# Performance work log

Hardware: AMD Instinct MI355X
Metric: run time of the kernel (lower is better)

The kernel has to match this reference:

```python
import jax, jax.numpy as jnp
import numpy as np

N = 8192
FEAT = 3
TRIG = 2
SA = 2
H = 64
ACT = 3
NEG = -1.0e9
EPS = 1e-5


def setup_inputs() -> dict:
    key = jax.random.key(0)
    ks = jax.random.split(key, 24)
    s = 0.05
    node_features = jax.random.uniform(ks[0], (N, FEAT), dtype=jnp.float32)
    adj = jax.random.randint(ks[1], (N, N), 0, 2).astype(jnp.float32)
    # ensure self-loops so every row has at least one neighbor
    adj_matrix = jnp.maximum(adj, jnp.eye(N, dtype=jnp.float32))
    trigger_context = jax.random.uniform(ks[2], (TRIG,), dtype=jnp.float32)
    sa_priors = jax.random.normal(ks[3], (N, SA), dtype=jnp.float32)
    p = lambda k, sh: jax.random.normal(k, sh, dtype=jnp.float32) * s
    return {
        "node_features": node_features,
        "adj_matrix": adj_matrix,
        "trigger_context": trigger_context,
        "sa_priors": sa_priors,
        # node_encoder: Linear(5,64) -> ReLU -> Linear(64,64)
        "w1": p(ks[4], (FEAT + TRIG, H)), "b1": jnp.zeros((H,), jnp.float32),
        "w2": p(ks[5], (H, H)), "b2": jnp.zeros((H,), jnp.float32),
        "wq": p(ks[6], (H, H)), "bq": jnp.zeros((H,), jnp.float32),
        "wk": p(ks[7], (H, H)), "bk": jnp.zeros((H,), jnp.float32),
        "wg": p(ks[8], (TRIG, H)), "bg": jnp.zeros((H,), jnp.float32),
        "stateful_bias": jnp.zeros((1,), jnp.float32),
        "wm": p(ks[9], (H, H)), "bm": jnp.zeros((H,), jnp.float32),
        "ln_g": jnp.ones((H,), jnp.float32), "ln_b": jnp.zeros((H,), jnp.float32),
        "wa1": p(ks[10], (H + SA, H)), "ba1": jnp.zeros((H,), jnp.float32),
        "wa2": p(ks[11], (H, ACT)), "ba2": jnp.zeros((ACT,), jnp.float32),
    }


def reference(node_features, adj_matrix, trigger_context, sa_priors,
              w1, b1, w2, b2, wq, bq, wk, bk, wg, bg, stateful_bias,
              wm, bm, ln_g, ln_b, wa1, ba1, wa2, ba2):
    n = node_features.shape[0]
    trig = jnp.broadcast_to(trigger_context[None, :], (n, TRIG))
    x = jnp.concatenate([node_features, trig], axis=1)          # [N, 5]
    h = jax.nn.relu(x @ w1 + b1) @ w2 + b2                       # [N, H]
    q = h @ wq + bq
    k = h @ wk + bk
    scores = (q @ k.T) * (1.0 / np.sqrt(H))                      # [N, N]
    gate_factor = jnp.mean(jax.nn.sigmoid(trigger_context @ wg + bg))
    topo = jnp.where(adj_matrix == 0, jnp.float32(NEG), adj_matrix)
    is_stateful = node_features[:, 2]
    is_reactive = 1.0 - trigger_context[0]
    sb = jnp.outer(is_stateful, is_stateful) * (stateful_bias[0] * is_reactive)
    scores = scores * gate_factor + topo + sb
    attn = jax.nn.softmax(scores, axis=1)                        # [N, N]
    messages = h @ wm + bm
    aggregated = attn @ messages                                 # [N, H]
    z = h + aggregated
    mu = jnp.mean(z, axis=-1, keepdims=True)
    var = jnp.mean(jnp.square(z - mu), axis=-1, keepdims=True)
    emb = (z - mu) * jax.lax.rsqrt(var + EPS) * ln_g + ln_b      # LayerNorm
    ai = jnp.concatenate([emb, sa_priors], axis=1)               # [N, H+2]
    q_values = jax.nn.relu(ai @ wa1 + ba1) @ wa2 + ba2           # [N, 3]
    return q_values
```

## Files before the change

kernel.cpp:

```cpp
#include <hip/hip_runtime.h>
#include <hip/hip_bf16.h>
#include <math.h>

#define N 8192
#define NEGV -1000000000.0f
#define EPSV 1e-05f
#define NSPLIT 4
#define CPS (N / NSPLIT)
#define NTILE (CPS / 64)

typedef short bf16x8 __attribute__((ext_vector_type(8)));
typedef float f32x4 __attribute__((ext_vector_type(4)));
typedef unsigned short u16;

#define WS_SCAL 0
#define WS_H    64
#define WS_ST   (WS_H + N * 64)
#define WS_SBI  (WS_ST + N)
#define WS_DEN  (WS_SBI + N)
#define WS_AGG  (WS_DEN + NSPLIT * N)
#define WS_F_END (WS_AGG + NSPLIT * N * 64)
#define WU_BASE (WS_F_END * 2)
#define WU_QB (WU_BASE)
#define WU_KB (WU_BASE + N * 64)
#define WU_MB (WU_BASE + 2 * N * 64)
#define WU_MT (WU_BASE + 3 * N * 64)

static __device__ __forceinline__ u16 f2bf(float f) {
    __hip_bfloat16 h = __float2bfloat16(f);
    return *(u16*)&h;
}

__global__ void prep_k(const float* __restrict__ tc, const float* __restrict__ wg,
                       const float* __restrict__ bg, const float* __restrict__ sbias,
                       float* __restrict__ scal) {
    int j = threadIdx.x;
    float v = tc[0] * wg[j] + tc[1] * wg[64 + j] + bg[j];
    float g = 1.0f / (1.0f + __expf(-v));
    for (int off = 32; off; off >>= 1) g += __shfl_xor(g, off, 64);
    if (j == 0) {
        scal[0] = 0.125f * (g * (1.0f / 64.0f));
        scal[1] = sbias[0] * (1.0f - tc[0]);
    }
}

__global__ __launch_bounds__(256) void embed_k(
    const float* __restrict__ nf, const float* __restrict__ tc,
    const float* __restrict__ w1, const float* __restrict__ b1,
    const float* __restrict__ w2, const float* __restrict__ b2,
    const float* __restrict__ wq, const float* __restrict__ bq,
    const float* __restrict__ wk, const float* __restrict__ bk,
    const float* __restrict__ wm, const float* __restrict__ bm,
    float* __restrict__ ws)
{
    const int w = threadIdx.x >> 6, lane = threadIdx.x & 63;
    const int row = blockIdx.x * 4 + w;
    __shared__ float ts[4][64], hs[4][64];
    const float qscale = ws[WS_SCAL + 0];
    const float coef   = ws[WS_SCAL + 1];
    const float f0 = nf[row * 3], f1 = nf[row * 3 + 1], f2 = nf[row * 3 + 2];
    const float t0 = tc[0], t1 = tc[1];
    float v = b1[lane];
    v = fmaf(f0, w1[lane], v);
    v = fmaf(f1, w1[64 + lane], v);
    v = fmaf(f2, w1[128 + lane], v);
    v = fmaf(t0, w1[192 + lane], v);
    v = fmaf(t1, w1[256 + lane], v);
    ts[w][lane] = fmaxf(v, 0.0f);
    __syncthreads();
    float hv = b2[lane];
    #pragma unroll 8
    for (int j = 0; j < 64; j++) hv = fmaf(ts[w][j], w2[j * 64 + lane], hv);
    hs[w][lane] = hv;
    ws[WS_H + row * 64 + lane] = hv;
    __syncthreads();
    float qv = bq[lane], kv = bk[lane], mv = bm[lane];
    #pragma unroll 4
    for (int j = 0; j < 64; j++) {
        const float hj = hs[w][j];
        qv = fmaf(hj, wq[j * 64 + lane], qv);
        kv = fmaf(hj, wk[j * 64 + lane], kv);
        mv = fmaf(hj, wm[j * 64 + lane], mv);
    }
    u16* wu = (u16*)ws;
    wu[WU_QB + row * 64 + lane] = f2bf(qv * qscale);
    wu[WU_KB + row * 64 + lane] = f2bf(kv);
    wu[WU_MB + row * 64 + lane] = f2bf(mv);
    if (lane == 0) {
        ws[WS_ST + row]  = f2;
        ws[WS_SBI + row] = f2 * coef;
    }
}

__global__ __launch_bounds__(256) void transp_k(float* __restrict__ ws) {
    const u16* mb = (const u16*)ws + WU_MB;
    u16* mt = (u16*)ws + WU_MT;
    __shared__ __align__(16) u16 tile[64][72];
    const int i0 = blockIdx.x * 64;
    const int t = threadIdx.x;
    {
        const int r = t >> 2, cb = (t & 3) * 16;
        *(uint4*)&tile[r][cb]     = *(const uint4*)&mb[(size_t)(i0 + r) * 64 + cb];
        *(uint4*)&tile[r][cb + 8] = *(const uint4*)&mb[(size_t)(i0 + r) * 64 + cb + 8];
    }
    __syncthreads();
    const int c = t >> 2, rb = (t & 3) * 16;
    u16 tmp[16];
    #pragma unroll
    for (int i = 0; i < 16; i++) tmp[i] = tile[rb + i][c];
    *(uint4*)&mt[(size_t)c * N + i0 + rb]     = *(uint4*)&tmp[0];
    *(uint4*)&mt[(size_t)c * N + i0 + rb + 8] = *(uint4*)&tmp[8];
}

__global__ __launch_bounds__(256, 2) void attn_k(const float* __restrict__ adj,
                                                 float* __restrict__ ws)
{
    const int rb = blockIdx.x, sp = blockIdx.y;
    const int i0 = rb * 64, j0 = sp * CPS;
    const int tid = threadIdx.x;
    const int w = tid >> 6, lane = tid & 63;
    const int quad = lane >> 4, n16 = lane & 15;
    const int m0 = w * 16;

    __shared__ __align__(16) u16 qs[64][72];
    __shared__ __align__(16) u16 ks[2][64][72];
    __shared__ __align__(16) u16 ms[2][64][72];
    __shared__ __align__(16) u16 ps[64][72];
    __shared__ float sts[2][64];
    __shared__ float sbis[64];

    const u16* qb = (const u16*)ws + WU_QB;
    const u16* kb = (const u16*)ws + WU_KB;
    const u16* mt = (const u16*)ws + WU_MT;

    const int sr = tid >> 2, scb = (tid & 3) * 16;

    *(uint4*)&qs[sr][scb]     = *(const uint4*)&qb[(size_t)(i0 + sr) * 64 + scb];
    *(uint4*)&qs[sr][scb + 8] = *(const uint4*)&qb[(size_t)(i0 + sr) * 64 + scb + 8];
    if (tid < 64) sbis[tid] = ws[WS_SBI + i0 + tid];
    {
        const int jt = j0;
        *(uint4*)&ks[0][sr][scb]     = *(const uint4*)&kb[(size_t)(jt + sr) * 64 + scb];
        *(uint4*)&ks[0][sr][scb + 8] = *(const uint4*)&kb[(size_t)(jt + sr) * 64 + scb + 8];
        *(uint4*)&ms[0][sr][scb]     = *(const uint4*)&mt[(size_t)sr * N + jt + scb];
        *(uint4*)&ms[0][sr][scb + 8] = *(const uint4*)&mt[(size_t)sr * N + jt + scb + 8];
        if (tid < 64) sts[0][tid] = ws[WS_ST + jt + tid];
    }
    __syncthreads();

    const bf16x8 aq0 = *(const bf16x8*)&qs[m0 + n16][quad * 8];
    const bf16x8 aq1 = *(const bf16x8*)&qs[m0 + n16][32 + quad * 8];

    f32x4 acc[4];
    #pragma unroll
    for (int i = 0; i < 4; i++) acc[i] = (f32x4){0.f, 0.f, 0.f, 0.f};
    float den[4] = {0.f, 0.f, 0.f, 0.f};
    float sbr[4];
    #pragma unroll
    for (int v = 0; v < 4; v++) sbr[v] = sbis[m0 + quad * 4 + v];

    for (int t = 0; t < NTILE; t++) {
        const int cur = t & 1;
        const int jt = j0 + t * 64;

        float aa[4][4];
        #pragma unroll
        for (int reg = 0; reg < 4; reg++) {
            const size_t rowb = (size_t)(i0 + m0 + quad * 4 + reg) * N + jt + n16;
            #pragma unroll
            for (int ct = 0; ct < 4; ct++) aa[ct][reg] = adj[rowb + ct * 16];
        }

        if (t + 1 < NTILE) {
            const int jn = jt + 64;
            *(uint4*)&ks[cur ^ 1][sr][scb]     = *(const uint4*)&kb[(size_t)(jn + sr) * 64 + scb];
            *(uint4*)&ks[cur ^ 1][sr][scb + 8] = *(const uint4*)&kb[(size_t)(jn + sr) * 64 + scb + 8];
            *(uint4*)&ms[cur ^ 1][sr][scb]     = *(const uint4*)&mt[(size_t)sr * N + jn + scb];
            *(uint4*)&ms[cur ^ 1][sr][scb + 8] = *(const uint4*)&mt[(size_t)sr * N + jn + scb + 8];
            if (tid < 64) sts[cur ^ 1][tid] = ws[WS_ST + jn + tid];
        }

        #pragma unroll
        for (int ct = 0; ct < 4; ct++) {
            const bf16x8 b0 = *(const bf16x8*)&ks[cur][ct * 16 + n16][quad * 8];
            const bf16x8 b1 = *(const bf16x8*)&ks[cur][ct * 16 + n16][32 + quad * 8];
            f32x4 s = {0.f, 0.f, 0.f, 0.f};
            s = __builtin_amdgcn_mfma_f32_16x16x32_bf16(aq0, b0, s, 0, 0, 0);
            s = __builtin_amdgcn_mfma_f32_16x16x32_bf16(aq1, b1, s, 0, 0, 0);
            const float stc = sts[cur][ct * 16 + n16];
            #pragma unroll
            for (int reg = 0; reg < 4; reg++) {
                const float a = aa[ct][reg];
                const float sc = s[reg] + (a == 0.0f ? NEGV : a) + sbr[reg] * stc;
                const float p = __expf(sc);
                den[reg] += p;
                ps[m0 + quad * 4 + reg][ct * 16 + n16] = f2bf(p);
            }
        }
        __syncthreads();

        const bf16x8 ap0 = *(const bf16x8*)&ps[m0 + n16][quad * 8];
        const bf16x8 ap1 = *(const bf16x8*)&ps[m0 + n16][32 + quad * 8];
        #pragma unroll
        for (int nt = 0; nt < 4; nt++) {
            const bf16x8 b0 = *(const bf16x8*)&ms[cur][nt * 16 + n16][quad * 8];
            const bf16x8 b1 = *(const bf16x8*)&ms[cur][nt * 16 + n16][32 + quad * 8];
            acc[nt] = __builtin_amdgcn_mfma_f32_16x16x32_bf16(ap0, b0, acc[nt], 0, 0, 0);
            acc[nt] = __builtin_amdgcn_mfma_f32_16x16x32_bf16(ap1, b1, acc[nt], 0, 0, 0);
        }
        __syncthreads();
    }

    float* aggp = ws + WS_AGG + (size_t)sp * N * 64;
    #pragma unroll
    for (int nt = 0; nt < 4; nt++) {
        #pragma unroll
        for (int reg = 0; reg < 4; reg++) {
            aggp[(size_t)(i0 + m0 + quad * 4 + reg) * 64 + nt * 16 + n16] = acc[nt][reg];
        }
    }
    #pragma unroll
    for (int reg = 0; reg < 4; reg++) {
        float d = den[reg];
        d += __shfl_xor(d, 1, 64);
        d += __shfl_xor(d, 2, 64);
        d += __shfl_xor(d, 4, 64);
        d += __shfl_xor(d, 8, 64);
        if (n16 == 0) ws[WS_DEN + sp * N + i0 + m0 + quad * 4 + reg] = d;
    }
}

__global__ __launch_bounds__(256) void final_k(
    const float* __restrict__ sa, const float* __restrict__ ln_g,
    const float* __restrict__ ln_b,
    const float* __restrict__ wa1, const float* __restrict__ ba1,
    const float* __restrict__ wa2, const float* __restrict__ ba2,
    const float* __restrict__ ws, float* __restrict__ out)
{
    const int w = threadIdx.x >> 6, lane = threadIdx.x & 63;
    const int row = blockIdx.x * 4 + w;
    __shared__ float es[4][64], hs2[4][64];
    float a = 0.0f;
    #pragma unroll
    for (int sp = 0; sp < NSPLIT; sp++)
        a += ws[WS_AGG + (size_t)sp * N * 64 + (size_t)row * 64 + lane];
    float d = 0.0f;
    #pragma unroll
    for (int sp = 0; sp < NSPLIT; sp++) d += ws[WS_DEN + sp * N + row];
    const float z = ws[WS_H + row * 64 + lane] + a / d;
    float mu = z;
    for (int off = 32; off; off >>= 1) mu += __shfl_xor(mu, off, 64);
    mu *= (1.0f / 64.0f);
    const float zc = z - mu;
    float var = zc * zc;
    for (int off = 32; off; off >>= 1) var += __shfl_xor(var, off, 64);
    var *= (1.0f / 64.0f);
    const float emb = zc * rsqrtf(var + EPSV) * ln_g[lane] + ln_b[lane];
    es[w][lane] = emb;
    __syncthreads();
    const float sa0 = sa[row * 2], sa1 = sa[row * 2 + 1];
    float hv = ba1[lane];
    #pragma unroll 8
    for (int c = 0; c < 64; c++) hv = fmaf(es[w][c], wa1[c * 64 + lane], hv);
    hv = fmaf(sa0, wa1[64 * 64 + lane], hv);
    hv = fmaf(sa1, wa1[65 * 64 + lane], hv);
    hs2[w][lane] = fmaxf(hv, 0.0f);
    __syncthreads();
    if (lane < 3) {
        float o = ba2[lane];
        for (int u = 0; u < 64; u++) o = fmaf(hs2[w][u], wa2[u * 3 + lane], o);
        out[row * 3 + lane] = o;
    }
}

extern "C" void kernel_launch(void* const* d_in, const int* in_sizes, int n_in,
                              void* d_out, int out_size, void* d_ws, size_t ws_size,
                              hipStream_t stream)
{
    const float* nf  = (const float*)d_in[0];
    const float* adj = (const float*)d_in[1];
    const float* tc  = (const float*)d_in[2];
    const float* sa  = (const float*)d_in[3];
    const float* w1  = (const float*)d_in[4];
    const float* b1  = (const float*)d_in[5];
    const float* w2  = (const float*)d_in[6];
    const float* b2  = (const float*)d_in[7];
    const float* wq  = (const float*)d_in[8];
    const float* bq  = (const float*)d_in[9];
    const float* wk  = (const float*)d_in[10];
    const float* bk  = (const float*)d_in[11];
    const float* wg  = (const float*)d_in[12];
    const float* bg  = (const float*)d_in[13];
    const float* sb  = (const float*)d_in[14];
    const float* wm  = (const float*)d_in[15];
    const float* bm  = (const float*)d_in[16];
    const float* lng = (const float*)d_in[17];
    const float* lnb = (const float*)d_in[18];
    const float* wa1 = (const float*)d_in[19];
    const float* ba1 = (const float*)d_in[20];
    const float* wa2 = (const float*)d_in[21];
    const float* ba2 = (const float*)d_in[22];
    float* ws  = (float*)d_ws;
    float* out = (float*)d_out;

    prep_k<<<1, 64, 0, stream>>>(tc, wg, bg, sb, ws + WS_SCAL);
    embed_k<<<N / 4, 256, 0, stream>>>(nf, tc, w1, b1, w2, b2, wq, bq, wk, bk,
                                       wm, bm, ws);
    transp_k<<<N / 64, 256, 0, stream>>>(ws);
    attn_k<<<dim3(N / 64, NSPLIT), 256, 0, stream>>>(adj, ws);
    final_k<<<N / 4, 256, 0, stream>>>(sa, lng, lnb, wa1, ba1, wa2, ba2, ws, out);
}
```

Measured before the change: 474.2 us.

## Register-prefetch K/M and adjacency tiles, single-buffer LDS, double the column splits

```diff
diff --git a/kernel.cpp b/kernel.cpp
--- a/kernel.cpp
+++ b/kernel.cpp
@@ -5,7 +5,7 @@
 #define N 8192
 #define NEGV -1000000000.0f
 #define EPSV 1e-05f
-#define NSPLIT 4
+#define NSPLIT 8
 #define CPS (N / NSPLIT)
 #define NTILE (CPS / 64)
 
@@ -112,85 +112,102 @@
     *(uint4*)&mt[(size_t)c * N + i0 + rb + 8] = *(uint4*)&tmp[8];
 }
 
-__global__ __launch_bounds__(256, 2) void attn_k(const float* __restrict__ adj,
+__global__ __launch_bounds__(256, 3) void attn_k(const float* __restrict__ adj,
                                                  float* __restrict__ ws)
 {
     const int rb = blockIdx.x, sp = blockIdx.y;
     const int i0 = rb * 64, j0 = sp * CPS;
     const int tid = threadIdx.x;
-    const int w = tid >> 6, lane = tid & 63;
+    const int lane = tid & 63;
     const int quad = lane >> 4, n16 = lane & 15;
-    const int m0 = w * 16;
-
-    __shared__ __align__(16) u16 qs[64][72];
-    __shared__ __align__(16) u16 ks[2][64][72];
-    __shared__ __align__(16) u16 ms[2][64][72];
+    const int m0 = (tid >> 6) * 16;
+
+    __shared__ __align__(16) u16 ks[64][72];
+    __shared__ __align__(16) u16 ms[64][72];
     __shared__ __align__(16) u16 ps[64][72];
-    __shared__ float sts[2][64];
-    __shared__ float sbis[64];
 
     const u16* qb = (const u16*)ws + WU_QB;
     const u16* kb = (const u16*)ws + WU_KB;
     const u16* mt = (const u16*)ws + WU_MT;
+    const float* st_g = ws + WS_ST;
 
     const int sr = tid >> 2, scb = (tid & 3) * 16;
 
-    *(uint4*)&qs[sr][scb]     = *(const uint4*)&qb[(size_t)(i0 + sr) * 64 + scb];
-    *(uint4*)&qs[sr][scb + 8] = *(const uint4*)&qb[(size_t)(i0 + sr) * 64 + scb + 8];
-    if (tid < 64) sbis[tid] = ws[WS_SBI + i0 + tid];
+    uint4 kmA[2][4];
+    float aaR[2][4][4];
+    float stR[2][4];
+
     {
         const int jt = j0;
-        *(uint4*)&ks[0][sr][scb]     = *(const uint4*)&kb[(size_t)(jt + sr) * 64 + scb];
-        *(uint4*)&ks[0][sr][scb + 8] = *(const uint4*)&kb[(size_t)(jt + sr) * 64 + scb + 8];
-        *(uint4*)&ms[0][sr][scb]     = *(const uint4*)&mt[(size_t)sr * N + jt + scb];
-        *(uint4*)&ms[0][sr][scb + 8] = *(const uint4*)&mt[(size_t)sr * N + jt + scb + 8];
-        if (tid < 64) sts[0][tid] = ws[WS_ST + jt + tid];
-    }
-    __syncthreads();
-
-    const bf16x8 aq0 = *(const bf16x8*)&qs[m0 + n16][quad * 8];
-    const bf16x8 aq1 = *(const bf16x8*)&qs[m0 + n16][32 + quad * 8];
-
-    f32x4 acc[4];
-    #pragma unroll
-    for (int i = 0; i < 4; i++) acc[i] = (f32x4){0.f, 0.f, 0.f, 0.f};
-    float den[4] = {0.f, 0.f, 0.f, 0.f};
-    float sbr[4];
-    #pragma unroll
-    for (int v = 0; v < 4; v++) sbr[v] = sbis[m0 + quad * 4 + v];
-
-    for (int t = 0; t < NTILE; t++) {
-        const int cur = t & 1;
-        const int jt = j0 + t * 64;
-
-        float aa[4][4];
+        uint4 k0 = *(const uint4*)&kb[(size_t)(jt + sr) * 64 + scb];
+        uint4 k1 = *(const uint4*)&kb[(size_t)(jt + sr) * 64 + scb + 8];
+        uint4 q0 = *(const uint4*)&mt[(size_t)sr * N + jt + scb];
+        uint4 q1 = *(const uint4*)&mt[(size_t)sr * N + jt + scb + 8];
         #pragma unroll
         for (int reg = 0; reg < 4; reg++) {
             const size_t rowb = (size_t)(i0 + m0 + quad * 4 + reg) * N + jt + n16;
             #pragma unroll
-            for (int ct = 0; ct < 4; ct++) aa[ct][reg] = adj[rowb + ct * 16];
-        }
-
-        if (t + 1 < NTILE) {
-            const int jn = jt + 64;
-            *(uint4*)&ks[cur ^ 1][sr][scb]     = *(const uint4*)&kb[(size_t)(jn + sr) * 64 + scb];
-            *(uint4*)&ks[cur ^ 1][sr][scb + 8] = *(const uint4*)&kb[(size_t)(jn + sr) * 64 + scb + 8];
-            *(uint4*)&ms[cur ^ 1][sr][scb]     = *(const uint4*)&mt[(size_t)sr * N + jn + scb];
-            *(uint4*)&ms[cur ^ 1][sr][scb + 8] = *(const uint4*)&mt[(size_t)sr * N + jn + scb + 8];
-            if (tid < 64) sts[cur ^ 1][tid] = ws[WS_ST + jn + tid];
+            for (int ct = 0; ct < 4; ct++) aaR[0][ct][reg] = adj[rowb + ct * 16];
+        }
+        #pragma unroll
+        for (int ct = 0; ct < 4; ct++) stR[0][ct] = st_g[jt + ct * 16 + n16];
+        const int j1 = j0 + ((NTILE > 1) ? 64 : 0);
+        kmA[1][0] = *(const uint4*)&kb[(size_t)(j1 + sr) * 64 + scb];
+        kmA[1][1] = *(const uint4*)&kb[(size_t)(j1 + sr) * 64 + scb + 8];
+        kmA[1][2] = *(const uint4*)&mt[(size_t)sr * N + j1 + scb];
+        kmA[1][3] = *(const uint4*)&mt[(size_t)sr * N + j1 + scb + 8];
+        *(uint4*)&ks[sr][scb]     = k0;
+        *(uint4*)&ks[sr][scb + 8] = k1;
+        *(uint4*)&ms[sr][scb]     = q0;
+        *(uint4*)&ms[sr][scb + 8] = q1;
+    }
+
+    const bf16x8 aq0 = *(const bf16x8*)&qb[(size_t)(i0 + m0 + n16) * 64 + quad * 8];
+    const bf16x8 aq1 = *(const bf16x8*)&qb[(size_t)(i0 + m0 + n16) * 64 + 32 + quad * 8];
+    float sbr[4];
+    #pragma unroll
+    for (int v = 0; v < 4; v++) sbr[v] = ws[WS_SBI + i0 + m0 + quad * 4 + v];
+
+    f32x4 acc[4];
+    #pragma unroll
+    for (int i = 0; i < 4; i++) acc[i] = (f32x4){0.f, 0.f, 0.f, 0.f};
+    float den[4] = {0.f, 0.f, 0.f, 0.f};
+
+    __syncthreads();
+
+    #pragma unroll 2
+    for (int t = 0; t < NTILE; t++) {
+        const int cur = t & 1, nxt = 1 - cur;
+        {
+            const int tk = (t + 2 < NTILE) ? t + 2 : NTILE - 1;
+            const int jk = j0 + tk * 64;
+            kmA[cur][0] = *(const uint4*)&kb[(size_t)(jk + sr) * 64 + scb];
+            kmA[cur][1] = *(const uint4*)&kb[(size_t)(jk + sr) * 64 + scb + 8];
+            kmA[cur][2] = *(const uint4*)&mt[(size_t)sr * N + jk + scb];
+            kmA[cur][3] = *(const uint4*)&mt[(size_t)sr * N + jk + scb + 8];
+            const int ta = (t + 1 < NTILE) ? t + 1 : NTILE - 1;
+            const int ja = j0 + ta * 64;
+            #pragma unroll
+            for (int reg = 0; reg < 4; reg++) {
+                const size_t rowb = (size_t)(i0 + m0 + quad * 4 + reg) * N + ja + n16;
+                #pragma unroll
+                for (int ct = 0; ct < 4; ct++) aaR[nxt][ct][reg] = adj[rowb + ct * 16];
+            }
+            #pragma unroll
+            for (int ct = 0; ct < 4; ct++) stR[nxt][ct] = st_g[ja + ct * 16 + n16];
         }
 
         #pragma unroll
         for (int ct = 0; ct < 4; ct++) {
-            const bf16x8 b0 = *(const bf16x8*)&ks[cur][ct * 16 + n16][quad * 8];
-            const bf16x8 b1 = *(const bf16x8*)&ks[cur][ct * 16 + n16][32 + quad * 8];
+            const bf16x8 b0 = *(const bf16x8*)&ks[ct * 16 + n16][quad * 8];
+            const bf16x8 b1 = *(const bf16x8*)&ks[ct * 16 + n16][32 + quad * 8];
             f32x4 s = {0.f, 0.f, 0.f, 0.f};
             s = __builtin_amdgcn_mfma_f32_16x16x32_bf16(aq0, b0, s, 0, 0, 0);
             s = __builtin_amdgcn_mfma_f32_16x16x32_bf16(aq1, b1, s, 0, 0, 0);
-            const float stc = sts[cur][ct * 16 + n16];
+            const float stc = stR[cur][ct];
             #pragma unroll
             for (int reg = 0; reg < 4; reg++) {
-                const float a = aa[ct][reg];
+                const float a = aaR[cur][ct][reg];
                 const float sc = s[reg] + (a == 0.0f ? NEGV : a) + sbr[reg] * stc;
                 const float p = __expf(sc);
                 den[reg] += p;
@@ -203,11 +220,17 @@
         const bf16x8 ap1 = *(const bf16x8*)&ps[m0 + n16][32 + quad * 8];
         #pragma unroll
         for (int nt = 0; nt < 4; nt++) {
-            const bf16x8 b0 = *(const bf16x8*)&ms[cur][nt * 16 + n16][quad * 8];
-            const bf16x8 b1 = *(const bf16x8*)&ms[cur][nt * 16 + n16][32 + quad * 8];
+            const bf16x8 b0 = *(const bf16x8*)&ms[nt * 16 + n16][quad * 8];
+            const bf16x8 b1 = *(const bf16x8*)&ms[nt * 16 + n16][32 + quad * 8];
             acc[nt] = __builtin_amdgcn_mfma_f32_16x16x32_bf16(ap0, b0, acc[nt], 0, 0, 0);
             acc[nt] = __builtin_amdgcn_mfma_f32_16x16x32_bf16(ap1, b1, acc[nt], 0, 0, 0);
         }
+        __syncthreads();
+
+        *(uint4*)&ks[sr][scb]     = kmA[nxt][0];
+        *(uint4*)&ks[sr][scb + 8] = kmA[nxt][1];
+        *(uint4*)&ms[sr][scb]     = kmA[nxt][2];
+        *(uint4*)&ms[sr][scb + 8] = kmA[nxt][3];
         __syncthreads();
     }
 
```

After: 553.6 us. +16.7%, slower.

## Register-prefetch next adjacency tile and K/M tiles to overlap loads with MFMA

Applied to the files above, without the earlier changes.

```diff
diff --git a/kernel.cpp b/kernel.cpp
--- a/kernel.cpp
+++ b/kernel.cpp
@@ -5,7 +5,7 @@
 #define N 8192
 #define NEGV -1000000000.0f
 #define EPSV 1e-05f
-#define NSPLIT 4
+#define NSPLIT 8
 #define CPS (N / NSPLIT)
 #define NTILE (CPS / 64)
 
@@ -112,103 +112,118 @@
     *(uint4*)&mt[(size_t)c * N + i0 + rb + 8] = *(uint4*)&tmp[8];
 }
 
-__global__ __launch_bounds__(256, 2) void attn_k(const float* __restrict__ adj,
+#define TILE_BODY(CUR, ADJ_RD, ST_RD, ADJ_WR, ST_WR)                          \
+{                                                                             \
+    const int jn = (jt + 64 < jend) ? (jt + 64) : jt;                         \
+    _Pragma("unroll")                                                         \
+    for (int reg = 0; reg < 4; reg++) {                                       \
+        const size_t rowb = (size_t)(i0 + m0 + quad * 4 + reg) * N + jn + n16;\
+        _Pragma("unroll")                                                     \
+        for (int ct = 0; ct < 4; ct++) ADJ_WR[ct][reg] = adj[rowb + ct * 16]; \
+    }                                                                         \
+    _Pragma("unroll")                                                         \
+    for (int ct = 0; ct < 4; ct++) ST_WR[ct] = st_g[jn + ct * 16 + n16];      \
+    const uint4 kn0 = *(const uint4*)&kb[(size_t)(jn + sr) * 64 + scb];       \
+    const uint4 kn1 = *(const uint4*)&kb[(size_t)(jn + sr) * 64 + scb + 8];   \
+    const uint4 mn0 = *(const uint4*)&mt[(size_t)sr * N + jn + scb];          \
+    const uint4 mn1 = *(const uint4*)&mt[(size_t)sr * N + jn + scb + 8];      \
+    _Pragma("unroll")                                                         \
+    for (int ct = 0; ct < 4; ct++) {                                          \
+        const bf16x8 b0 = *(const bf16x8*)&ks[CUR][ct * 16 + n16][quad * 8];  \
+        const bf16x8 b1 = *(const bf16x8*)&ks[CUR][ct * 16 + n16][32 + quad * 8]; \
+        f32x4 s = {0.f, 0.f, 0.f, 0.f};                                       \
+        s = __builtin_amdgcn_mfma_f32_16x16x32_bf16(aq0, b0, s, 0, 0, 0);     \
+        s = __builtin_amdgcn_mfma_f32_16x16x32_bf16(aq1, b1, s, 0, 0, 0);     \
+        const float stc = ST_RD[ct];                                          \
+        _Pragma("unroll")                                                     \
+        for (int reg = 0; reg < 4; reg++) {                                   \
+            const float a = ADJ_RD[ct][reg];                                  \
+            const float sc = s[reg] + (a == 0.0f ? NEGV : a) + sbr[reg] * stc;\
+            const float p = __expf(sc);                                       \
+            den[reg] += p;                                                    \
+            ps[m0 + quad * 4 + reg][ct * 16 + n16] = f2bf(p);                 \
+        }                                                                     \
+    }                                                                         \
+    __syncthreads();                                                          \
+    {                                                                         \
+        const bf16x8 ap0 = *(const bf16x8*)&ps[m0 + n16][quad * 8];           \
+        const bf16x8 ap1 = *(const bf16x8*)&ps[m0 + n16][32 + quad * 8];      \
+        _Pragma("unroll")                                                     \
+        for (int nt = 0; nt < 4; nt++) {                                      \
+            const bf16x8 b0 = *(const bf16x8*)&ms[CUR][nt * 16 + n16][quad * 8]; \
+            const bf16x8 b1 = *(const bf16x8*)&ms[CUR][nt * 16 + n16][32 + quad * 8]; \
+            acc[nt] = __builtin_amdgcn_mfma_f32_16x16x32_bf16(ap0, b0, acc[nt], 0, 0, 0); \
+            acc[nt] = __builtin_amdgcn_mfma_f32_16x16x32_bf16(ap1, b1, acc[nt], 0, 0, 0); \
+        }                                                                     \
+    }                                                                         \
+    *(uint4*)&ks[1 - (CUR)][sr][scb]     = kn0;                               \
+    *(uint4*)&ks[1 - (CUR)][sr][scb + 8] = kn1;                               \
+    *(uint4*)&ms[1 - (CUR)][sr][scb]     = mn0;                               \
+    *(uint4*)&ms[1 - (CUR)][sr][scb + 8] = mn1;                               \
+    __syncthreads();                                                          \
+    jt += 64;                                                                 \
+}
+
+__global__ __launch_bounds__(256, 3) void attn_k(const float* __restrict__ adj,
                                                  float* __restrict__ ws)
 {
     const int rb = blockIdx.x, sp = blockIdx.y;
     const int i0 = rb * 64, j0 = sp * CPS;
+    const int jend = j0 + CPS;
     const int tid = threadIdx.x;
-    const int w = tid >> 6, lane = tid & 63;
+    const int lane = tid & 63;
     const int quad = lane >> 4, n16 = lane & 15;
-    const int m0 = w * 16;
-
-    __shared__ __align__(16) u16 qs[64][72];
+    const int m0 = (tid >> 6) * 16;
+
     __shared__ __align__(16) u16 ks[2][64][72];
     __shared__ __align__(16) u16 ms[2][64][72];
-    __shared__ __align__(16) u16 ps[64][72];
-    __shared__ float sts[2][64];
-    __shared__ float sbis[64];
+    __shared__ __align__(16) u16 ps[64][76];
 
     const u16* qb = (const u16*)ws + WU_QB;
     const u16* kb = (const u16*)ws + WU_KB;
     const u16* mt = (const u16*)ws + WU_MT;
+    const float* st_g = ws + WS_ST;
 
     const int sr = tid >> 2, scb = (tid & 3) * 16;
 
-    *(uint4*)&qs[sr][scb]     = *(const uint4*)&qb[(size_t)(i0 + sr) * 64 + scb];
-    *(uint4*)&qs[sr][scb + 8] = *(const uint4*)&qb[(size_t)(i0 + sr) * 64 + scb + 8];
-    if (tid < 64) sbis[tid] = ws[WS_SBI + i0 + tid];
+    float adjA[4][4], adjB[4][4], stA[4], stB[4];
+
+    #pragma unroll
+    for (int reg = 0; reg < 4; reg++) {
+        const size_t rowb = (size_t)(i0 + m0 + quad * 4 + reg) * N + j0 + n16;
+        #pragma unroll
+        for (int ct = 0; ct < 4; ct++) adjA[ct][reg] = adj[rowb + ct * 16];
+    }
+    #pragma unroll
+    for (int ct = 0; ct < 4; ct++) stA[ct] = st_g[j0 + ct * 16 + n16];
     {
-        const int jt = j0;
-        *(uint4*)&ks[0][sr][scb]     = *(const uint4*)&kb[(size_t)(jt + sr) * 64 + scb];
-        *(uint4*)&ks[0][sr][scb + 8] = *(const uint4*)&kb[(size_t)(jt + sr) * 64 + scb + 8];
-        *(uint4*)&ms[0][sr][scb]     = *(const uint4*)&mt[(size_t)sr * N + jt + scb];
-        *(uint4*)&ms[0][sr][scb + 8] = *(const uint4*)&mt[(size_t)sr * N + jt + scb + 8];
-        if (tid < 64) sts[0][tid] = ws[WS_ST + jt + tid];
-    }
-    __syncthreads();
-
-    const bf16x8 aq0 = *(const bf16x8*)&qs[m0 + n16][quad * 8];
-    const bf16x8 aq1 = *(const bf16x8*)&qs[m0 + n16][32 + quad * 8];
+        const uint4 k0 = *(const uint4*)&kb[(size_t)(j0 + sr) * 64 + scb];
+        const uint4 k1 = *(const uint4*)&kb[(size_t)(j0 + sr) * 64 + scb + 8];
+        const uint4 q0 = *(const uint4*)&mt[(size_t)sr * N + j0 + scb];
+        const uint4 q1 = *(const uint4*)&mt[(size_t)sr * N + j0 + scb + 8];
+        *(uint4*)&ks[0][sr][scb]     = k0;
+        *(uint4*)&ks[0][sr][scb + 8] = k1;
+        *(uint4*)&ms[0][sr][scb]     = q0;
+        *(uint4*)&ms[0][sr][scb + 8] = q1;
+    }
+
+    const bf16x8 aq0 = *(const bf16x8*)&qb[(size_t)(i0 + m0 + n16) * 64 + quad * 8];
+    const bf16x8 aq1 = *(const bf16x8*)&qb[(size_t)(i0 + m0 + n16) * 64 + 32 + quad * 8];
+    float sbr[4];
+    #pragma unroll
+    for (int v = 0; v < 4; v++) sbr[v] = ws[WS_SBI + i0 + m0 + quad * 4 + v];
 
     f32x4 acc[4];
     #pragma unroll
     for (int i = 0; i < 4; i++) acc[i] = (f32x4){0.f, 0.f, 0.f, 0.f};
     float den[4] = {0.f, 0.f, 0.f, 0.f};
-    float sbr[4];
-    #pragma unroll
-    for (int v = 0; v < 4; v++) sbr[v] = sbis[m0 + quad * 4 + v];
-
-    for (int t = 0; t < NTILE; t++) {
-        const int cur = t & 1;
-        const int jt = j0 + t * 64;
-
-        float aa[4][4];
-        #pragma unroll
-        for (int reg = 0; reg < 4; reg++) {
-            const size_t rowb = (size_t)(i0 + m0 + quad * 4 + reg) * N + jt + n16;
-            #pragma unroll
-            for (int ct = 0; ct < 4; ct++) aa[ct][reg] = adj[rowb + ct * 16];
-        }
-
-        if (t + 1 < NTILE) {
-            const int jn = jt + 64;
-            *(uint4*)&ks[cur ^ 1][sr][scb]     = *(const uint4*)&kb[(size_t)(jn + sr) * 64 + scb];
-            *(uint4*)&ks[cur ^ 1][sr][scb + 8] = *(const uint4*)&kb[(size_t)(jn + sr) * 64 + scb + 8];
-            *(uint4*)&ms[cur ^ 1][sr][scb]     = *(const uint4*)&mt[(size_t)sr * N + jn + scb];
-            *(uint4*)&ms[cur ^ 1][sr][scb + 8] = *(const uint4*)&mt[(size_t)sr * N + jn + scb + 8];
-            if (tid < 64) sts[cur ^ 1][tid] = ws[WS_ST + jn + tid];
-        }
-
-        #pragma unroll
-        for (int ct = 0; ct < 4; ct++) {
-            const bf16x8 b0 = *(const bf16x8*)&ks[cur][ct * 16 + n16][quad * 8];
-            const bf16x8 b1 = *(const bf16x8*)&ks[cur][ct * 16 + n16][32 + quad * 8];
-            f32x4 s = {0.f, 0.f, 0.f, 0.f};
-            s = __builtin_amdgcn_mfma_f32_16x16x32_bf16(aq0, b0, s, 0, 0, 0);
-            s = __builtin_amdgcn_mfma_f32_16x16x32_bf16(aq1, b1, s, 0, 0, 0);
-            const float stc = sts[cur][ct * 16 + n16];
-            #pragma unroll
-            for (int reg = 0; reg < 4; reg++) {
-                const float a = aa[ct][reg];
-                const float sc = s[reg] + (a == 0.0f ? NEGV : a) + sbr[reg] * stc;
-                const float p = __expf(sc);
-                den[reg] += p;
-                ps[m0 + quad * 4 + reg][ct * 16 + n16] = f2bf(p);
-            }
-        }
-        __syncthreads();
-
-        const bf16x8 ap0 = *(const bf16x8*)&ps[m0 + n16][quad * 8];
-        const bf16x8 ap1 = *(const bf16x8*)&ps[m0 + n16][32 + quad * 8];
-        #pragma unroll
-        for (int nt = 0; nt < 4; nt++) {
-            const bf16x8 b0 = *(const bf16x8*)&ms[cur][nt * 16 + n16][quad * 8];
-            const bf16x8 b1 = *(const bf16x8*)&ms[cur][nt * 16 + n16][32 + quad * 8];
-            acc[nt] = __builtin_amdgcn_mfma_f32_16x16x32_bf16(ap0, b0, acc[nt], 0, 0, 0);
-            acc[nt] = __builtin_amdgcn_mfma_f32_16x16x32_bf16(ap1, b1, acc[nt], 0, 0, 0);
-        }
-        __syncthreads();
+
+    __syncthreads();
+
+    int jt = j0;
+    for (int t = 0; t < NTILE; t += 2) {
+        TILE_BODY(0, adjA, stA, adjB, stB)
+        TILE_BODY(1, adjB, stB, adjA, stA)
     }
 
     float* aggp = ws + WS_AGG + (size_t)sp * N * 64;
```

After: 491.6 us. +3.7%, slower.

## Pre-swizzle K/M into MFMA fragment layout and stream attention operands from global

Applied to the files above, without the earlier changes.

```diff
diff --git a/kernel.cpp b/kernel.cpp
--- a/kernel.cpp
+++ b/kernel.cpp
@@ -5,7 +5,7 @@
 #define N 8192
 #define NEGV -1000000000.0f
 #define EPSV 1e-05f
-#define NSPLIT 4
+#define NSPLIT 8
 #define CPS (N / NSPLIT)
 #define NTILE (CPS / 64)
 
@@ -22,9 +22,9 @@
 #define WS_F_END (WS_AGG + NSPLIT * N * 64)
 #define WU_BASE (WS_F_END * 2)
 #define WU_QB (WU_BASE)
-#define WU_KB (WU_BASE + N * 64)
+#define WU_KF (WU_BASE + N * 64)
 #define WU_MB (WU_BASE + 2 * N * 64)
-#define WU_MT (WU_BASE + 3 * N * 64)
+#define WU_MF (WU_BASE + 3 * N * 64)
 
 static __device__ __forceinline__ u16 f2bf(float f) {
     __hip_bfloat16 h = __float2bfloat16(f);
@@ -84,7 +84,13 @@
     }
     u16* wu = (u16*)ws;
     wu[WU_QB + row * 64 + lane] = f2bf(qv * qscale);
-    wu[WU_KB + row * 64 + lane] = f2bf(kv);
+    {
+        const size_t kb4 = row >> 6;
+        const int ct = row & 3, n16r = (row & 63) >> 2;
+        const int half = lane >> 5, quadl = (lane >> 3) & 3, jl = lane & 7;
+        const size_t flat = ((((kb4 * 4 + ct) * 2 + half) * 4 + quadl) * 16 + n16r) * 8 + jl;
+        wu[WU_KF + flat] = f2bf(kv);
+    }
     wu[WU_MB + row * 64 + lane] = f2bf(mv);
     if (lane == 0) {
         ws[WS_ST + row]  = f2;
@@ -92,123 +98,106 @@
     }
 }
 
-__global__ __launch_bounds__(256) void transp_k(float* __restrict__ ws) {
+__global__ __launch_bounds__(256) void mfrag_k(float* __restrict__ ws) {
     const u16* mb = (const u16*)ws + WU_MB;
-    u16* mt = (u16*)ws + WU_MT;
+    u16* mf = (u16*)ws + WU_MF;
     __shared__ __align__(16) u16 tile[64][72];
-    const int i0 = blockIdx.x * 64;
+    const int jb = blockIdx.x;
     const int t = threadIdx.x;
     {
         const int r = t >> 2, cb = (t & 3) * 16;
-        *(uint4*)&tile[r][cb]     = *(const uint4*)&mb[(size_t)(i0 + r) * 64 + cb];
-        *(uint4*)&tile[r][cb + 8] = *(const uint4*)&mb[(size_t)(i0 + r) * 64 + cb + 8];
-    }
-    __syncthreads();
-    const int c = t >> 2, rb = (t & 3) * 16;
-    u16 tmp[16];
-    #pragma unroll
-    for (int i = 0; i < 16; i++) tmp[i] = tile[rb + i][c];
-    *(uint4*)&mt[(size_t)c * N + i0 + rb]     = *(uint4*)&tmp[0];
-    *(uint4*)&mt[(size_t)c * N + i0 + rb + 8] = *(uint4*)&tmp[8];
-}
-
-__global__ __launch_bounds__(256, 2) void attn_k(const float* __restrict__ adj,
+        *(uint4*)&tile[r][cb]     = *(const uint4*)&mb[(size_t)(jb * 64 + r) * 64 + cb];
+        *(uint4*)&tile[r][cb + 8] = *(const uint4*)&mb[(size_t)(jb * 64 + r) * 64 + cb + 8];
+    }
+    __syncthreads();
+    #pragma unroll
+    for (int cc = 0; cc < 2; cc++) {
+        const int c = t * 2 + cc;
+        const int n16 = c & 15, quad = (c >> 4) & 3;
+        const int half = (c >> 6) & 1, nt = c >> 7;
+        u16 tmp[8];
+        #pragma unroll
+        for (int j = 0; j < 8; j++) tmp[j] = tile[half * 32 + quad * 8 + j][nt * 16 + n16];
+        *(uint4*)&mf[(size_t)jb * 4096 + (size_t)c * 8] = *(uint4*)&tmp[0];
+    }
+}
+
+__global__ __launch_bounds__(256, 4) void attn_k(const float* __restrict__ adj,
                                                  float* __restrict__ ws)
 {
     const int rb = blockIdx.x, sp = blockIdx.y;
     const int i0 = rb * 64, j0 = sp * CPS;
     const int tid = threadIdx.x;
-    const int w = tid >> 6, lane = tid & 63;
+    const int lane = tid & 63;
     const int quad = lane >> 4, n16 = lane & 15;
-    const int m0 = w * 16;
-
-    __shared__ __align__(16) u16 qs[64][72];
-    __shared__ __align__(16) u16 ks[2][64][72];
-    __shared__ __align__(16) u16 ms[2][64][72];
-    __shared__ __align__(16) u16 ps[64][72];
-    __shared__ float sts[2][64];
-    __shared__ float sbis[64];
+    const int m0 = (tid >> 6) * 16;
+
+    __shared__ __align__(16) u16 ps[64][76];
 
     const u16* qb = (const u16*)ws + WU_QB;
-    const u16* kb = (const u16*)ws + WU_KB;
-    const u16* mt = (const u16*)ws + WU_MT;
-
-    const int sr = tid >> 2, scb = (tid & 3) * 16;
-
-    *(uint4*)&qs[sr][scb]     = *(const uint4*)&qb[(size_t)(i0 + sr) * 64 + scb];
-    *(uint4*)&qs[sr][scb + 8] = *(const uint4*)&qb[(size_t)(i0 + sr) * 64 + scb + 8];
-    if (tid < 64) sbis[tid] = ws[WS_SBI + i0 + tid];
-    {
-        const int jt = j0;
-        *(uint4*)&ks[0][sr][scb]     = *(const uint4*)&kb[(size_t)(jt + sr) * 64 + scb];
-        *(uint4*)&ks[0][sr][scb + 8] = *(const uint4*)&kb[(size_t)(jt + sr) * 64 + scb + 8];
-        *(uint4*)&ms[0][sr][scb]     = *(const uint4*)&mt[(size_t)sr * N + jt + scb];
-        *(uint4*)&ms[0][sr][scb + 8] = *(const uint4*)&mt[(size_t)sr * N + jt + scb + 8];
-        if (tid < 64) sts[0][tid] = ws[WS_ST + jt + tid];
-    }
-    __syncthreads();
-
-    const bf16x8 aq0 = *(const bf16x8*)&qs[m0 + n16][quad * 8];
-    const bf16x8 aq1 = *(const bf16x8*)&qs[m0 + n16][32 + quad * 8];
+    const u16* kf = (const u16*)ws + WU_KF;
+    const u16* mf = (const u16*)ws + WU_MF;
+    const float* st_g = ws + WS_ST;
+
+    const bf16x8 aq0 = *(const bf16x8*)&qb[(size_t)(i0 + m0 + n16) * 64 + quad * 8];
+    const bf16x8 aq1 = *(const bf16x8*)&qb[(size_t)(i0 + m0 + n16) * 64 + 32 + quad * 8];
+    float sbr[4];
+    #pragma unroll
+    for (int v = 0; v < 4; v++) sbr[v] = ws[WS_SBI + i0 + m0 + quad * 4 + v];
 
     f32x4 acc[4];
     #pragma unroll
     for (int i = 0; i < 4; i++) acc[i] = (f32x4){0.f, 0.f, 0.f, 0.f};
     float den[4] = {0.f, 0.f, 0.f, 0.f};
-    float sbr[4];
-    #pragma unroll
-    for (int v = 0; v < 4; v++) sbr[v] = sbis[m0 + quad * 4 + v];
-
+
+    const int fragoff = (quad * 16 + n16) * 8;
+
+    #pragma unroll 2
     for (int t = 0; t < NTILE; t++) {
-        const int cur = t & 1;
         const int jt = j0 + t * 64;
-
-        float aa[4][4];
+        const u16* kfb = kf + (size_t)(jt >> 6) * 4096;
+        const u16* mfb = mf + (size_t)(jt >> 6) * 4096;
+
+        float4 aa[4];
+        #pragma unroll
+        for (int reg = 0; reg < 4; reg++)
+            aa[reg] = *(const float4*)&adj[(size_t)(i0 + m0 + quad * 4 + reg) * N + jt + n16 * 4];
+        const float4 st4 = *(const float4*)&st_g[jt + n16 * 4];
+
+        f32x4 s[4];
+        #pragma unroll
+        for (int ct = 0; ct < 4; ct++) {
+            const bf16x8 b0 = *(const bf16x8*)&kfb[(ct * 2 + 0) * 512 + fragoff];
+            const bf16x8 b1 = *(const bf16x8*)&kfb[(ct * 2 + 1) * 512 + fragoff];
+            f32x4 sv = {0.f, 0.f, 0.f, 0.f};
+            sv = __builtin_amdgcn_mfma_f32_16x16x32_bf16(aq0, b0, sv, 0, 0, 0);
+            sv = __builtin_amdgcn_mfma_f32_16x16x32_bf16(aq1, b1, sv, 0, 0, 0);
+            s[ct] = sv;
+        }
+
         #pragma unroll
         for (int reg = 0; reg < 4; reg++) {
-            const size_t rowb = (size_t)(i0 + m0 + quad * 4 + reg) * N + jt + n16;
-            #pragma unroll
-            for (int ct = 0; ct < 4; ct++) aa[ct][reg] = adj[rowb + ct * 16];
+            const float sb_r = sbr[reg];
+            float a0 = aa[reg].x, a1 = aa[reg].y, a2 = aa[reg].z, a3 = aa[reg].w;
+            const float p0 = __expf(s[0][reg] + (a0 == 0.0f ? NEGV : a0) + sb_r * st4.x);
+            const float p1 = __expf(s[1][reg] + (a1 == 0.0f ? NEGV : a1) + sb_r * st4.y);
+            const float p2 = __expf(s[2][reg] + (a2 == 0.0f ? NEGV : a2) + sb_r * st4.z);
+            const float p3 = __expf(s[3][reg] + (a3 == 0.0f ? NEGV : a3) + sb_r * st4.w);
+            den[reg] += (p0 + p1) + (p2 + p3);
+            ushort4 pw;
+            pw.x = f2bf(p0); pw.y = f2bf(p1); pw.z = f2bf(p2); pw.w = f2bf(p3);
+            *(ushort4*)&ps[m0 + quad * 4 + reg][n16 * 4] = pw;
         }
-
-        if (t + 1 < NTILE) {
-            const int jn = jt + 64;
-            *(uint4*)&ks[cur ^ 1][sr][scb]     = *(const uint4*)&kb[(size_t)(jn + sr) * 64 + scb];
-            *(uint4*)&ks[cur ^ 1][sr][scb + 8] = *(const uint4*)&kb[(size_t)(jn + sr) * 64 + scb + 8];
-            *(uint4*)&ms[cur ^ 1][sr][scb]     = *(const uint4*)&mt[(size_t)sr * N + jn + scb];
-            *(uint4*)&ms[cur ^ 1][sr][scb + 8] = *(const uint4*)&mt[(size_t)sr * N + jn + scb + 8];
-            if (tid < 64) sts[cur ^ 1][tid] = ws[WS_ST + jn + tid];
-        }
-
-        #pragma unroll
-        for (int ct = 0; ct < 4; ct++) {
-            const bf16x8 b0 = *(const bf16x8*)&ks[cur][ct * 16 + n16][quad * 8];
-            const bf16x8 b1 = *(const bf16x8*)&ks[cur][ct * 16 + n16][32 + quad * 8];
-            f32x4 s = {0.f, 0.f, 0.f, 0.f};
-            s = __builtin_amdgcn_mfma_f32_16x16x32_bf16(aq0, b0, s, 0, 0, 0);
-            s = __builtin_amdgcn_mfma_f32_16x16x32_bf16(aq1, b1, s, 0, 0, 0);
-            const float stc = sts[cur][ct * 16 + n16];
-            #pragma unroll
-            for (int reg = 0; reg < 4; reg++) {
-                const float a = aa[ct][reg];
-                const float sc = s[reg] + (a == 0.0f ? NEGV : a) + sbr[reg] * stc;
-                const float p = __expf(sc);
-                den[reg] += p;
-                ps[m0 + quad * 4 + reg][ct * 16 + n16] = f2bf(p);
-            }
-        }
-        __syncthreads();
 
         const bf16x8 ap0 = *(const bf16x8*)&ps[m0 + n16][quad * 8];
         const bf16x8 ap1 = *(const bf16x8*)&ps[m0 + n16][32 + quad * 8];
         #pragma unroll
         for (int nt = 0; nt < 4; nt++) {
-            const bf16x8 b0 = *(const bf16x8*)&ms[cur][nt * 16 + n16][quad * 8];
-            const bf16x8 b1 = *(const bf16x8*)&ms[cur][nt * 16 + n16][32 + quad * 8];
+            const bf16x8 b0 = *(const bf16x8*)&mfb[(nt * 2 + 0) * 512 + fragoff];
+            const bf16x8 b1 = *(const bf16x8*)&mfb[(nt * 2 + 1) * 512 + fragoff];
             acc[nt] = __builtin_amdgcn_mfma_f32_16x16x32_bf16(ap0, b0, acc[nt], 0, 0, 0);
             acc[nt] = __builtin_amdgcn_mfma_f32_16x16x32_bf16(ap1, b1, acc[nt], 0, 0, 0);
         }
-        __syncthreads();
     }
 
     float* aggp = ws + WS_AGG + (size_t)sp * N * 64;
@@ -306,7 +295,7 @@
     prep_k<<<1, 64, 0, stream>>>(tc, wg, bg, sb, ws + WS_SCAL);
     embed_k<<<N / 4, 256, 0, stream>>>(nf, tc, w1, b1, w2, b2, wq, bq, wk, bk,
                                        wm, bm, ws);
-    transp_k<<<N / 64, 256, 0, stream>>>(ws);
+    mfrag_k<<<N / 64, 256, 0, stream>>>(ws);
     attn_k<<<dim3(N / 64, NSPLIT), 256, 0, stream>>>(adj, ws);
     final_k<<<N / 4, 256, 0, stream>>>(sa, lng, lnb, wa1, ba1, wa2, ba2, ws, out);
 }
```

Result: slower. 502.5 us (+6.0%).
